# Optimization experiments

Hardware: AMD Instinct MI355X
Metric: run time of the kernel (lower is better)

The kernel has to match this reference:

```python
import jax, jax.numpy as jnp
import numpy as np

N_NODES = 100000
N_EDGES = 1600000


def gcn_conv(x, edge_index, W, b, num_nodes):
    # PyG GCNConv (normalize=True, add_self_loops=True):
    #   out = D^{-1/2} (A + I) D^{-1/2} (x @ W) + b
    h = x @ W  # [N, out_ch]
    src = jnp.concatenate([edge_index[0], jnp.arange(num_nodes, dtype=edge_index.dtype)])
    dst = jnp.concatenate([edge_index[1], jnp.arange(num_nodes, dtype=edge_index.dtype)])
    deg = jax.ops.segment_sum(jnp.ones_like(dst, dtype=h.dtype), dst, num_segments=num_nodes)
    dinv = jnp.where(deg > 0, jax.lax.rsqrt(deg), 0.0)  # deg^{-1/2}, inf->0
    norm = dinv[src] * dinv[dst]  # [E+N]
    msgs = h[src] * norm[:, None]  # gather + scale, [E+N, out_ch]
    out = jax.ops.segment_sum(msgs, dst, num_segments=num_nodes)
    return out + b


def setup_inputs() -> dict:
    key = jax.random.key(0)
    kx, ke, kw1, kw2 = jax.random.split(key, 4)
    x = jax.random.normal(kx, (N_NODES, 32), dtype=jnp.float32)
    edge_index = jax.random.randint(ke, (2, N_EDGES), 0, N_NODES, dtype=jnp.int64)
    W1 = jax.random.normal(kw1, (32, 64), dtype=jnp.float32) * (1.0 / np.sqrt(32))
    b1 = jnp.zeros((64,), dtype=jnp.float32)
    W2 = jax.random.normal(kw2, (64, 64), dtype=jnp.float32) * (1.0 / np.sqrt(64))
    b2 = jnp.zeros((64,), dtype=jnp.float32)
    return {"x": x, "edge_index": edge_index, "W1": W1, "b1": b1, "W2": W2, "b2": b2}


def reference(x, edge_index, W1, b1, W2, b2):
    n = x.shape[0]
    h = jax.nn.relu(gcn_conv(x, edge_index, W1, b1, n))
    h = jax.nn.relu(gcn_conv(h, edge_index, W2, b2, n))
    return h
```

## Files before the change

### kernel.cpp

```cpp
#include <hip/hip_runtime.h>

#define N_NODES 100000
#define N_EDGES 1600000
#define BSHIFT 9
#define BNODES 512
#define NB ((N_NODES + BNODES - 1) / BNODES)
#define NBP 256
#define NHB 256
#define TILE 4096
#define EPT 16

typedef _Float16 half8 __attribute__((ext_vector_type(8)));
typedef _Float16 half4 __attribute__((ext_vector_type(4)));
typedef float floatx4 __attribute__((ext_vector_type(4)));


__global__ __launch_bounds__(256) void k_hist(const int* __restrict__ dst,
                                              int* __restrict__ partial, int e) {
    __shared__ int h[NBP];
    for (int i = threadIdx.x; i < NBP; i += 256) h[i] = 0;
    __syncthreads();
    int chunk = (e + NHB - 1) / NHB;
    int lo = blockIdx.x * chunk;
    int hi = min(e, lo + chunk);
    for (int i = lo + threadIdx.x; i < hi; i += 256)
        atomicAdd(&h[dst[i] >> BSHIFT], 1);
    __syncthreads();
    for (int i = threadIdx.x; i < NBP; i += 256)
        partial[blockIdx.x * NBP + i] = h[i];
}

__device__ void packW_dev(const float* __restrict__ W, _Float16* __restrict__ Wp, int IC) {
    int total = IC * 64;
    for (int idx = threadIdx.x; idx < total; idx += 256) {
        int j = idx & 7;
        int l = (idx >> 3) & 63;
        int cbks = idx >> 9;
        int cb = cbks & 3;
        int ks = cbks >> 2;
        int k = ks * 32 + (l >> 4) * 8 + j;
        int c = cb * 16 + (l & 15);
        Wp[idx] = (_Float16)W[k * 64 + c];
    }
}

__global__ __launch_bounds__(256) void k_bscan_pack(
        const int* __restrict__ partial, int* __restrict__ bucketBase, int* __restrict__ bucketCur,
        const float* __restrict__ W1, _Float16* __restrict__ Wp1,
        const float* __restrict__ W2, _Float16* __restrict__ Wp2) {
    if (blockIdx.x == 1) { packW_dev(W1, Wp1, 32); return; }
    if (blockIdx.x == 2) { packW_dev(W2, Wp2, 64); return; }
    __shared__ int a[NBP];
    int t = threadIdx.x;
    int cnt = 0;
    for (int b = 0; b < NHB; ++b) cnt += partial[b * NBP + t];
    a[t] = cnt;
    __syncthreads();
    for (int off = 1; off < NBP; off <<= 1) {
        int v = (t >= off) ? a[t - off] : 0;
        __syncthreads();
        a[t] += v;
        __syncthreads();
    }
    if (t < NB) {
        int incl = a[t];
        int excl = incl - cnt;
        bucketBase[t] = excl;
        bucketCur[t] = excl;
        if (t == NB - 1) bucketBase[NB] = incl;
    }
}

__global__ __launch_bounds__(256) void k_redistribute(
        const int* __restrict__ src, const int* __restrict__ dst,
        int* __restrict__ bucketCur, int* __restrict__ packed, int e) {
    __shared__ int cnt[NBP], base[NBP], gdelta[NBP], lcur[NBP], a[NBP];
    __shared__ int sorted[TILE];
    __shared__ int sdelta[TILE];
    int tileBase = blockIdx.x * TILE;
    int tileCnt = min(TILE, e - tileBase);
    int t = threadIdx.x;
    for (int i = t; i < NBP; i += 256) cnt[i] = 0;
    __syncthreads();
    int pk[EPT], bk[EPT];
#pragma unroll
    for (int k = 0; k < EPT; ++k) {
        int i = k * 256 + t;
        if (i < tileCnt) {
            int d = dst[tileBase + i];
            int s = src[tileBase + i];
            bk[k] = d >> BSHIFT;
            pk[k] = (s << BSHIFT) | (d & (BNODES - 1));
            atomicAdd(&cnt[bk[k]], 1);
        } else bk[k] = -1;
    }
    __syncthreads();
    a[t] = cnt[t];
    __syncthreads();
    for (int off = 1; off < NBP; off <<= 1) {
        int v = (t >= off) ? a[t - off] : 0;
        __syncthreads();
        a[t] += v;
        __syncthreads();
    }
    base[t] = a[t] - cnt[t];
    lcur[t] = base[t];
    if (t < NB && cnt[t] > 0)
        gdelta[t] = atomicAdd(&bucketCur[t], cnt[t]) - base[t];
    __syncthreads();
#pragma unroll
    for (int k = 0; k < EPT; ++k) {
        if (bk[k] >= 0) {
            int l = atomicAdd(&lcur[bk[k]], 1);
            sorted[l] = pk[k];
            sdelta[l] = gdelta[bk[k]];
        }
    }
    __syncthreads();
    for (int i = t; i < tileCnt; i += 256)
        packed[i + sdelta[i]] = sorted[i];
}

__global__ __launch_bounds__(512) void k_bucket_csr(
        const int* __restrict__ packed, const int* __restrict__ bucketBase,
        int* __restrict__ rowptr, int* __restrict__ col, float* __restrict__ dinv,
        int n, int e) {
    __shared__ int hist[BNODES], a[BNODES], cur[BNODES];
    int b = blockIdx.x;
    int node0 = b * BNODES;
    int nn = min(BNODES, n - node0);
    int eb = bucketBase[b], ee = bucketBase[b + 1];
    int t = threadIdx.x;
    hist[t] = 0;
    __syncthreads();
    for (int i = eb + t; i < ee; i += 512)
        atomicAdd(&hist[packed[i] & (BNODES - 1)], 1);
    __syncthreads();
    a[t] = hist[t];
    __syncthreads();
    for (int off = 1; off < BNODES; off <<= 1) {
        int v = (t >= off) ? a[t - off] : 0;
        __syncthreads();
        a[t] += v;
        __syncthreads();
    }
    int excl = a[t] - hist[t];
    cur[t] = excl;
    if (t < nn) {
        rowptr[node0 + t] = eb + excl;
        dinv[node0 + t] = rsqrtf((float)(1 + hist[t]));
    }
    if (b == gridDim.x - 1 && t == 0) rowptr[n] = e;
    __syncthreads();
    for (int i = eb + t; i < ee; i += 512) {
        int p = packed[i];
        int dl = p & (BNODES - 1);
        int l = atomicAdd(&cur[dl], 1);
        col[eb + l] = p >> BSHIFT;
    }
}


__global__ void k_prescale(const float* __restrict__ X, const float* __restrict__ dinv,
                           _Float16* __restrict__ U, int n) {
    int idx = blockIdx.x * blockDim.x + threadIdx.x;
    if (idx >= n * 8) return;
    int node = idx >> 3;
    float4 v = ((const float4*)X)[idx];
    float di = dinv[node];
    half4 h;
    h[0] = (_Float16)(v.x * di);
    h[1] = (_Float16)(v.y * di);
    h[2] = (_Float16)(v.z * di);
    h[3] = (_Float16)(v.w * di);
    ((half4*)U)[idx] = h;
}


template <int LPN>
__global__ void k_gatherh(const _Float16* __restrict__ G, const int* __restrict__ rowptr,
                          const int* __restrict__ col, const float* __restrict__ dinv,
                          _Float16* __restrict__ out, int n) {
    constexpr int RW = LPN;
    int idx = blockIdx.x * blockDim.x + threadIdx.x;
    int node = idx / LPN;
    int l = idx % LPN;
    if (node >= n) return;
    const half8* Gr = (const half8*)G;
    half8 s = Gr[(size_t)node * RW + l];
    float acc[8];
#pragma unroll
    for (int q = 0; q < 8; ++q) acc[q] = (float)s[q];
    int jb = rowptr[node], je = rowptr[node + 1];
    int j = jb;
    for (; j + 3 < je; j += 4) {
        int s0 = col[j], s1 = col[j + 1], s2 = col[j + 2], s3 = col[j + 3];
        half8 v0 = Gr[(size_t)s0 * RW + l];
        half8 v1 = Gr[(size_t)s1 * RW + l];
        half8 v2 = Gr[(size_t)s2 * RW + l];
        half8 v3 = Gr[(size_t)s3 * RW + l];
#pragma unroll
        for (int q = 0; q < 8; ++q)
            acc[q] += ((float)v0[q] + (float)v1[q]) + ((float)v2[q] + (float)v3[q]);
    }
    for (; j < je; ++j) {
        half8 v0 = Gr[(size_t)col[j] * RW + l];
#pragma unroll
        for (int q = 0; q < 8; ++q) acc[q] += (float)v0[q];
    }
    float di = dinv[node];
    half8 r;
#pragma unroll
    for (int q = 0; q < 8; ++q) r[q] = (_Float16)(acc[q] * di);
    ((half8*)out)[(size_t)node * RW + l] = r;
}


template <int IC, bool FP16OUT>
__global__ __launch_bounds__(256) void k_gemm_mfma(
        const _Float16* __restrict__ A, const _Float16* __restrict__ Wp,
        const float* __restrict__ bias, const float* __restrict__ dinv,
        void* __restrict__ outv, int n) {
    constexpr int KS = IC / 32;
    const int lane = threadIdx.x & 63;
    const int w = threadIdx.x >> 6;
    int tile = blockIdx.x * 4 + w;
    int node0 = tile * 16;
    if (node0 >= n) return;

    half8 bf[KS][4];
#pragma unroll
    for (int ks = 0; ks < KS; ++ks)
#pragma unroll
        for (int cb = 0; cb < 4; ++cb)
            bf[ks][cb] = ((const half8*)Wp)[(ks * 4 + cb) * 64 + lane];

    const _Float16* Ar = A + (size_t)(node0 + (lane & 15)) * IC + (lane >> 4) * 8;
    half8 af[KS];
#pragma unroll
    for (int ks = 0; ks < KS; ++ks)
        af[ks] = *(const half8*)(Ar + ks * 32);

    floatx4 z = {0.f, 0.f, 0.f, 0.f};
    floatx4 acc[4] = {z, z, z, z};
#pragma unroll
    for (int ks = 0; ks < KS; ++ks)
#pragma unroll
        for (int cb = 0; cb < 4; ++cb)
            acc[cb] = __builtin_amdgcn_mfma_f32_16x16x32_f16(af[ks], bf[ks][cb], acc[cb], 0, 0, 0);

    int r0 = node0 + (lane >> 4) * 4;
    int ch0 = lane & 15;
    float di[4];
#pragma unroll
    for (int r = 0; r < 4; ++r) di[r] = FP16OUT ? dinv[r0 + r] : 0.f;
#pragma unroll
    for (int cb = 0; cb < 4; ++cb) {
        int ch = cb * 16 + ch0;
        float bb = bias[ch];
#pragma unroll
        for (int r = 0; r < 4; ++r) {
            float v = acc[cb][r] + bb;
            v = v > 0.f ? v : 0.f;
            if (FP16OUT)
                ((_Float16*)outv)[(size_t)(r0 + r) * 64 + ch] = (_Float16)(v * di[r]);
            else
                ((float*)outv)[(size_t)(r0 + r) * 64 + ch] = v;
        }
    }
}


extern "C" void kernel_launch(void* const* d_in, const int* in_sizes, int n_in,
                              void* d_out, int out_size, void* d_ws, size_t ws_size,
                              hipStream_t stream) {
    const float* x  = (const float*)d_in[0];
    const int* ei   = (const int*)d_in[1];
    const float* W1 = (const float*)d_in[2];
    const float* b1 = (const float*)d_in[3];
    const float* W2 = (const float*)d_in[4];
    const float* b2 = (const float*)d_in[5];

    const int N = N_NODES;
    const int E = N_EDGES;
    const int* src = ei;
    const int* dst = ei + E;

    char* ws = (char*)d_ws;
    size_t off = 0;
    auto alloc = [&](size_t bytes) { void* p = ws + off; off = (off + bytes + 511) & ~511ull; return p; };
    int*   partial    = (int*)  alloc((size_t)NHB * NBP * 4);
    int*   bucketBase = (int*)  alloc((size_t)(NB + 1) * 4);
    int*   bucketCur  = (int*)  alloc((size_t)NB * 4);
    int*   packed     = (int*)  alloc((size_t)E * 4);
    int*   rowptr     = (int*)  alloc((size_t)(N + 1) * 4);
    int*   col        = (int*)  alloc((size_t)E * 4);
    float* dinv       = (float*)alloc((size_t)N * 4);
    _Float16* Wp1     = (_Float16*)alloc((size_t)32 * 64 * 2);
    _Float16* Wp2     = (_Float16*)alloc((size_t)64 * 64 * 2);
    _Float16* slabA   = (_Float16*)alloc((size_t)N * 64 * 2);
    _Float16* xh1     = slabA;
    _Float16* agg1h   = slabA + (size_t)N * 32;
    _Float16* agg2h   = slabA;
    _Float16* xh2     = (_Float16*)alloc((size_t)N * 64 * 2);
    float* outF       = (float*)d_out;

    const int B = 256;
    const int nTiles = (E + TILE - 1) / TILE;
    const int nMfmaBlocks = (N / 16 + 3) / 4;

    k_hist<<<NHB, B, 0, stream>>>(dst, partial, E);
    k_bscan_pack<<<3, B, 0, stream>>>(partial, bucketBase, bucketCur, W1, Wp1, W2, Wp2);
    k_redistribute<<<nTiles, B, 0, stream>>>(src, dst, bucketCur, packed, E);
    k_bucket_csr<<<NB, BNODES, 0, stream>>>(packed, bucketBase, rowptr, col, dinv, N, E);

    k_prescale<<<(N * 8 + B - 1) / B, B, 0, stream>>>(x, dinv, xh1, N);

    k_gatherh<4><<<((size_t)N * 4 + B - 1) / B, B, 0, stream>>>(xh1, rowptr, col, dinv, agg1h, N);
    k_gemm_mfma<32, true><<<nMfmaBlocks, B, 0, stream>>>(agg1h, Wp1, b1, dinv, xh2, N);

    k_gatherh<8><<<((size_t)N * 8 + B - 1) / B, B, 0, stream>>>(xh2, rowptr, col, dinv, agg2h, N);
    k_gemm_mfma<64, false><<<nMfmaBlocks, B, 0, stream>>>(agg2h, Wp2, b2, dinv, outF, N);
}
```

Measured before the change: 127.9 us.

## Fuse prescale into CSR build and gather with MFMA GEMM per layer

The fp16 prescale of x is folded into the bucket CSR kernel, using a shared-memory copy of dinv. Each layer's neighbour gather and MFMA GEMM now run in one kernel that stages the aggregated 64-node tile in LDS. This removes three kernel launches and the global write and re-read of the aggregated intermediates. In exchange, the layer-2 gather uses half as many threads per node, each issuing two vector loads per edge, which may hide memory latency less well.

```diff
diff --git a/kernel.cpp b/kernel.cpp
--- a/kernel.cpp
+++ b/kernel.cpp
@@ -124,8 +124,10 @@
 __global__ __launch_bounds__(512) void k_bucket_csr(
         const int* __restrict__ packed, const int* __restrict__ bucketBase,
         int* __restrict__ rowptr, int* __restrict__ col, float* __restrict__ dinv,
+        const float* __restrict__ X, _Float16* __restrict__ xh1,
         int n, int e) {
     __shared__ int hist[BNODES], a[BNODES], cur[BNODES];
+    __shared__ float dinvS[BNODES];
     int b = blockIdx.x;
     int node0 = b * BNODES;
     int nn = min(BNODES, n - node0);
@@ -146,9 +148,11 @@
     }
     int excl = a[t] - hist[t];
     cur[t] = excl;
+    float di = rsqrtf((float)(1 + hist[t]));
+    dinvS[t] = di;
     if (t < nn) {
         rowptr[node0 + t] = eb + excl;
-        dinv[node0 + t] = rsqrtf((float)(1 + hist[t]));
+        dinv[node0 + t] = di;
     }
     if (b == gridDim.x - 1 && t == 0) rowptr[n] = e;
     __syncthreads();
@@ -158,114 +162,176 @@
         int l = atomicAdd(&cur[dl], 1);
         col[eb + l] = p >> BSHIFT;
     }
-}
-
-
-__global__ void k_prescale(const float* __restrict__ X, const float* __restrict__ dinv,
-                           _Float16* __restrict__ U, int n) {
-    int idx = blockIdx.x * blockDim.x + threadIdx.x;
-    if (idx >= n * 8) return;
-    int node = idx >> 3;
-    float4 v = ((const float4*)X)[idx];
-    float di = dinv[node];
-    half4 h;
-    h[0] = (_Float16)(v.x * di);
-    h[1] = (_Float16)(v.y * di);
-    h[2] = (_Float16)(v.z * di);
-    h[3] = (_Float16)(v.w * di);
-    ((half4*)U)[idx] = h;
-}
-
-
-template <int LPN>
-__global__ void k_gatherh(const _Float16* __restrict__ G, const int* __restrict__ rowptr,
-                          const int* __restrict__ col, const float* __restrict__ dinv,
-                          _Float16* __restrict__ out, int n) {
-    constexpr int RW = LPN;
-    int idx = blockIdx.x * blockDim.x + threadIdx.x;
-    int node = idx / LPN;
-    int l = idx % LPN;
-    if (node >= n) return;
-    const half8* Gr = (const half8*)G;
-    half8 s = Gr[(size_t)node * RW + l];
-    float acc[8];
-#pragma unroll
-    for (int q = 0; q < 8; ++q) acc[q] = (float)s[q];
-    int jb = rowptr[node], je = rowptr[node + 1];
-    int j = jb;
-    for (; j + 3 < je; j += 4) {
-        int s0 = col[j], s1 = col[j + 1], s2 = col[j + 2], s3 = col[j + 3];
-        half8 v0 = Gr[(size_t)s0 * RW + l];
-        half8 v1 = Gr[(size_t)s1 * RW + l];
-        half8 v2 = Gr[(size_t)s2 * RW + l];
-        half8 v3 = Gr[(size_t)s3 * RW + l];
-#pragma unroll
-        for (int q = 0; q < 8; ++q)
-            acc[q] += ((float)v0[q] + (float)v1[q]) + ((float)v2[q] + (float)v3[q]);
-    }
-    for (; j < je; ++j) {
-        half8 v0 = Gr[(size_t)col[j] * RW + l];
-#pragma unroll
-        for (int q = 0; q < 8; ++q) acc[q] += (float)v0[q];
-    }
-    float di = dinv[node];
-    half8 r;
-#pragma unroll
-    for (int q = 0; q < 8; ++q) r[q] = (_Float16)(acc[q] * di);
-    ((half8*)out)[(size_t)node * RW + l] = r;
-}
-
-
-template <int IC, bool FP16OUT>
-__global__ __launch_bounds__(256) void k_gemm_mfma(
-        const _Float16* __restrict__ A, const _Float16* __restrict__ Wp,
-        const float* __restrict__ bias, const float* __restrict__ dinv,
-        void* __restrict__ outv, int n) {
-    constexpr int KS = IC / 32;
-    const int lane = threadIdx.x & 63;
-    const int w = threadIdx.x >> 6;
-    int tile = blockIdx.x * 4 + w;
-    int node0 = tile * 16;
-    if (node0 >= n) return;
-
-    half8 bf[KS][4];
-#pragma unroll
-    for (int ks = 0; ks < KS; ++ks)
-#pragma unroll
-        for (int cb = 0; cb < 4; ++cb)
-            bf[ks][cb] = ((const half8*)Wp)[(ks * 4 + cb) * 64 + lane];
-
-    const _Float16* Ar = A + (size_t)(node0 + (lane & 15)) * IC + (lane >> 4) * 8;
-    half8 af[KS];
-#pragma unroll
-    for (int ks = 0; ks < KS; ++ks)
-        af[ks] = *(const half8*)(Ar + ks * 32);
-
-    floatx4 z = {0.f, 0.f, 0.f, 0.f};
-    floatx4 acc[4] = {z, z, z, z};
-#pragma unroll
-    for (int ks = 0; ks < KS; ++ks)
-#pragma unroll
-        for (int cb = 0; cb < 4; ++cb)
-            acc[cb] = __builtin_amdgcn_mfma_f32_16x16x32_f16(af[ks], bf[ks][cb], acc[cb], 0, 0, 0);
-
-    int r0 = node0 + (lane >> 4) * 4;
-    int ch0 = lane & 15;
-    float di[4];
-#pragma unroll
-    for (int r = 0; r < 4; ++r) di[r] = FP16OUT ? dinv[r0 + r] : 0.f;
-#pragma unroll
-    for (int cb = 0; cb < 4; ++cb) {
-        int ch = cb * 16 + ch0;
-        float bb = bias[ch];
-#pragma unroll
-        for (int r = 0; r < 4; ++r) {
-            float v = acc[cb][r] + bb;
-            v = v > 0.f ? v : 0.f;
-            if (FP16OUT)
-                ((_Float16*)outv)[(size_t)(r0 + r) * 64 + ch] = (_Float16)(v * di[r]);
-            else
-                ((float*)outv)[(size_t)(r0 + r) * 64 + ch] = v;
+    const float4* X4 = (const float4*)X;
+    half4* U4 = (half4*)xh1;
+    for (int i = t; i < nn * 8; i += 512) {
+        int nl = i >> 3;
+        float4 v = X4[(size_t)(node0 + nl) * 8 + (i & 7)];
+        float d2 = dinvS[nl];
+        half4 h;
+        h[0] = (_Float16)(v.x * d2);
+        h[1] = (_Float16)(v.y * d2);
+        h[2] = (_Float16)(v.z * d2);
+        h[3] = (_Float16)(v.w * d2);
+        U4[(size_t)(node0 + nl) * 8 + (i & 7)] = h;
+    }
+}
+
+
+__global__ __launch_bounds__(256) void k_fused1(
+        const _Float16* __restrict__ G, const int* __restrict__ rowptr,
+        const int* __restrict__ col, const float* __restrict__ dinv,
+        const _Float16* __restrict__ Wp, const float* __restrict__ bias,
+        _Float16* __restrict__ out, int n) {
+    __shared__ _Float16 aggS[64][40];
+    const int t = threadIdx.x;
+    const int node0 = blockIdx.x * 64;
+    {
+        int nl = t >> 2, l = t & 3;
+        int node = node0 + nl;
+        if (node < n) {
+            const half8* Gr = (const half8*)G;
+            half8 s = Gr[(size_t)node * 4 + l];
+            float acc[8];
+#pragma unroll
+            for (int q = 0; q < 8; ++q) acc[q] = (float)s[q];
+            int jb = rowptr[node], je = rowptr[node + 1];
+            int j = jb;
+            for (; j + 3 < je; j += 4) {
+                int s0 = col[j], s1 = col[j + 1], s2 = col[j + 2], s3 = col[j + 3];
+                half8 v0 = Gr[(size_t)s0 * 4 + l];
+                half8 v1 = Gr[(size_t)s1 * 4 + l];
+                half8 v2 = Gr[(size_t)s2 * 4 + l];
+                half8 v3 = Gr[(size_t)s3 * 4 + l];
+#pragma unroll
+                for (int q = 0; q < 8; ++q)
+                    acc[q] += ((float)v0[q] + (float)v1[q]) + ((float)v2[q] + (float)v3[q]);
+            }
+            for (; j < je; ++j) {
+                half8 v0 = Gr[(size_t)col[j] * 4 + l];
+#pragma unroll
+                for (int q = 0; q < 8; ++q) acc[q] += (float)v0[q];
+            }
+            float di = dinv[node];
+            half8 r;
+#pragma unroll
+            for (int q = 0; q < 8; ++q) r[q] = (_Float16)(acc[q] * di);
+            *(half8*)&aggS[nl][l * 8] = r;
+        }
+    }
+    __syncthreads();
+    {
+        const int lane = t & 63;
+        const int w = t >> 6;
+        int base = w * 16;
+        int nw0 = node0 + base;
+        if (nw0 >= n) return;
+        half8 af = *(const half8*)&aggS[base + (lane & 15)][(lane >> 4) * 8];
+        floatx4 z = {0.f, 0.f, 0.f, 0.f};
+        floatx4 acc[4] = {z, z, z, z};
+#pragma unroll
+        for (int cb = 0; cb < 4; ++cb) {
+            half8 bf = ((const half8*)Wp)[cb * 64 + lane];
+            acc[cb] = __builtin_amdgcn_mfma_f32_16x16x32_f16(af, bf, acc[cb], 0, 0, 0);
+        }
+        int r0 = nw0 + (lane >> 4) * 4;
+        int ch0 = lane & 15;
+        float di[4];
+#pragma unroll
+        for (int r = 0; r < 4; ++r) di[r] = dinv[r0 + r];
+#pragma unroll
+        for (int cb = 0; cb < 4; ++cb) {
+            int ch = cb * 16 + ch0;
+            float bb = bias[ch];
+#pragma unroll
+            for (int r = 0; r < 4; ++r) {
+                float v = acc[cb][r] + bb;
+                v = v > 0.f ? v : 0.f;
+                out[(size_t)(r0 + r) * 64 + ch] = (_Float16)(v * di[r]);
+            }
+        }
+    }
+}
+
+__global__ __launch_bounds__(256) void k_fused2(
+        const _Float16* __restrict__ G, const int* __restrict__ rowptr,
+        const int* __restrict__ col, const float* __restrict__ dinv,
+        const _Float16* __restrict__ Wp, const float* __restrict__ bias,
+        float* __restrict__ out, int n) {
+    __shared__ _Float16 aggS[64][72];
+    const int t = threadIdx.x;
+    const int node0 = blockIdx.x * 64;
+    {
+        int nl = t >> 2, l2 = (t & 3) * 2;
+        int node = node0 + nl;
+        if (node < n) {
+            const half8* Gr = (const half8*)G;
+            half8 sA = Gr[(size_t)node * 8 + l2];
+            half8 sB = Gr[(size_t)node * 8 + l2 + 1];
+            float accA[8], accB[8];
+#pragma unroll
+            for (int q = 0; q < 8; ++q) { accA[q] = (float)sA[q]; accB[q] = (float)sB[q]; }
+            int jb = rowptr[node], je = rowptr[node + 1];
+            int j = jb;
+            for (; j + 1 < je; j += 2) {
+                int s0 = col[j], s1 = col[j + 1];
+                half8 a0 = Gr[(size_t)s0 * 8 + l2];
+                half8 b0 = Gr[(size_t)s0 * 8 + l2 + 1];
+                half8 a1 = Gr[(size_t)s1 * 8 + l2];
+                half8 b1 = Gr[(size_t)s1 * 8 + l2 + 1];
+#pragma unroll
+                for (int q = 0; q < 8; ++q) {
+                    accA[q] += (float)a0[q] + (float)a1[q];
+                    accB[q] += (float)b0[q] + (float)b1[q];
+                }
+            }
+            if (j < je) {
+                int s0 = col[j];
+                half8 a0 = Gr[(size_t)s0 * 8 + l2];
+                half8 b0 = Gr[(size_t)s0 * 8 + l2 + 1];
+#pragma unroll
+                for (int q = 0; q < 8; ++q) { accA[q] += (float)a0[q]; accB[q] += (float)b0[q]; }
+            }
+            float di = dinv[node];
+            half8 rA, rB;
+#pragma unroll
+            for (int q = 0; q < 8; ++q) {
+                rA[q] = (_Float16)(accA[q] * di);
+                rB[q] = (_Float16)(accB[q] * di);
+            }
+            *(half8*)&aggS[nl][l2 * 8] = rA;
+            *(half8*)&aggS[nl][l2 * 8 + 8] = rB;
+        }
+    }
+    __syncthreads();
+    {
+        const int lane = t & 63;
+        const int w = t >> 6;
+        int base = w * 16;
+        int nw0 = node0 + base;
+        if (nw0 >= n) return;
+        half8 af0 = *(const half8*)&aggS[base + (lane & 15)][(lane >> 4) * 8];
+        half8 af1 = *(const half8*)&aggS[base + (lane & 15)][(lane >> 4) * 8 + 32];
+        floatx4 z = {0.f, 0.f, 0.f, 0.f};
+        floatx4 acc[4] = {z, z, z, z};
+#pragma unroll
+        for (int cb = 0; cb < 4; ++cb) {
+            half8 bf0 = ((const half8*)Wp)[(0 * 4 + cb) * 64 + lane];
+            half8 bf1 = ((const half8*)Wp)[(1 * 4 + cb) * 64 + lane];
+            acc[cb] = __builtin_amdgcn_mfma_f32_16x16x32_f16(af0, bf0, acc[cb], 0, 0, 0);
+            acc[cb] = __builtin_amdgcn_mfma_f32_16x16x32_f16(af1, bf1, acc[cb], 0, 0, 0);
+        }
+        int r0 = nw0 + (lane >> 4) * 4;
+        int ch0 = lane & 15;
+#pragma unroll
+        for (int cb = 0; cb < 4; ++cb) {
+            int ch = cb * 16 + ch0;
+            float bb = bias[ch];
+#pragma unroll
+            for (int r = 0; r < 4; ++r) {
+                float v = acc[cb][r] + bb;
+                out[(size_t)(r0 + r) * 64 + ch] = v > 0.f ? v : 0.f;
+            }
         }
     }
 }
@@ -298,27 +364,20 @@
     float* dinv       = (float*)alloc((size_t)N * 4);
     _Float16* Wp1     = (_Float16*)alloc((size_t)32 * 64 * 2);
     _Float16* Wp2     = (_Float16*)alloc((size_t)64 * 64 * 2);
-    _Float16* slabA   = (_Float16*)alloc((size_t)N * 64 * 2);
-    _Float16* xh1     = slabA;
-    _Float16* agg1h   = slabA + (size_t)N * 32;
-    _Float16* agg2h   = slabA;
+    _Float16* xh1     = (_Float16*)alloc((size_t)N * 32 * 2);
     _Float16* xh2     = (_Float16*)alloc((size_t)N * 64 * 2);
     float* outF       = (float*)d_out;
 
     const int B = 256;
     const int nTiles = (E + TILE - 1) / TILE;
-    const int nMfmaBlocks = (N / 16 + 3) / 4;
+    const int nFBlocks = (N + 63) / 64;
 
     k_hist<<<NHB, B, 0, stream>>>(dst, partial, E);
     k_bscan_pack<<<3, B, 0, stream>>>(partial, bucketBase, bucketCur, W1, Wp1, W2, Wp2);
     k_redistribute<<<nTiles, B, 0, stream>>>(src, dst, bucketCur, packed, E);
-    k_bucket_csr<<<NB, BNODES, 0, stream>>>(packed, bucketBase, rowptr, col, dinv, N, E);
-
-    k_prescale<<<(N * 8 + B - 1) / B, B, 0, stream>>>(x, dinv, xh1, N);
-
-    k_gatherh<4><<<((size_t)N * 4 + B - 1) / B, B, 0, stream>>>(xh1, rowptr, col, dinv, agg1h, N);
-    k_gemm_mfma<32, true><<<nMfmaBlocks, B, 0, stream>>>(agg1h, Wp1, b1, dinv, xh2, N);
-
-    k_gatherh<8><<<((size_t)N * 8 + B - 1) / B, B, 0, stream>>>(xh2, rowptr, col, dinv, agg2h, N);
-    k_gemm_mfma<64, false><<<nMfmaBlocks, B, 0, stream>>>(agg2h, Wp2, b2, dinv, outF, N);
-}
+    k_bucket_csr<<<NB, BNODES, 0, stream>>>(packed, bucketBase, rowptr, col, dinv, x, xh1, N, E);
+
+    k_fused1<<<nFBlocks, B, 0, stream>>>(xh1, rowptr, col, dinv, Wp1, b1, xh2, N);
+
+    k_fused2<<<nFBlocks, B, 0, stream>>>(xh2, rowptr, col, dinv, Wp2, b2, outF, N);
+}
```

Result: faster. 122.8 us (-4.0%).
